# Performance work log

Hardware: AMD Instinct MI355X
Metric: run time of the kernel (lower is better)

Reference implementation:

```python
import jax, jax.numpy as jnp
import numpy as np

B, S, E, HEADS = 2, 2048, 2048, 16


def setup_inputs() -> dict:
    key = jax.random.key(0)
    k1, k2, k3 = jax.random.split(key, 3)
    x = jax.random.normal(k1, (B, S, E), dtype=jnp.float32)
    # Linear weights stored as (in, out); torch uses y = x @ W.T with W (out, in) -- same math.
    W_qkvh = jax.random.normal(k2, (E, 3 * E + HEADS), dtype=jnp.float32) * (E ** -0.5)
    W_out = jax.random.normal(k3, (E, E), dtype=jnp.float32) * (E ** -0.5)
    return {"x": x, "W_qkvh": W_qkvh, "W_out": W_out}


def reference(x, W_qkvh, W_out):
    b, s, e = x.shape
    heads = W_qkvh.shape[1] - 3 * e
    d = e // heads
    scale = e ** 0.5

    proj = x @ W_qkvh                                  # (b, s, 3e + heads)
    QKV, Hg = proj[..., : 3 * e], proj[..., 3 * e:]
    Hg = jnp.tanh(Hg).transpose(0, 2, 1)[..., None]    # (b, h, s, 1) gate
    QKV = QKV.reshape(b, s, heads, 3 * d).transpose(0, 2, 1, 3)  # (b, h, s, 3d)
    Q, K, V = jnp.split(QKV, 3, axis=-1)               # each (b, h, s, d)

    # Cummean(H*K) along seq: cumsum(n * x) / n^2 with n = 1..s
    n = jnp.arange(1, s + 1, dtype=x.dtype).reshape(1, 1, s, 1)
    Kc = jnp.cumsum(n * (Hg * K), axis=2) / (n * n)    # (b, h, s, d)

    scores = jnp.einsum('bhqd,bhkd->bhqk', Q, Kc) / scale
    causal = jnp.triu(jnp.ones((s, s), dtype=bool), k=1)
    scores = jnp.where(causal, -jnp.inf, scores)
    attn = jax.nn.softmax(scores, axis=-1)

    out = jnp.einsum('bhqk,bhkd->bhqd', attn, V)       # (b, h, s, d)
    out = out.transpose(0, 2, 1, 3).reshape(b, s, e)
    return out @ W_out
```

## Files before the change

kernel.cpp:

```cpp
#include <hip/hip_runtime.h>
#include <hip/hip_bf16.h>
#include <math.h>

#define PB 2
#define PS 2048
#define PE 2048
#define PH 16
#define PD 128
#define PN_PROJ 6160
#define PM 4096
#define PQKV 6144

typedef __attribute__((ext_vector_type(8))) short bf16x8;
typedef __attribute__((ext_vector_type(4))) float f32x4;

__device__ __forceinline__ void gload_lds16(const void* g, void* l) {
  __builtin_amdgcn_global_load_lds((const __attribute__((address_space(1))) void*)g,
                                   (__attribute__((address_space(3))) void*)l, 16, 0, 0);
}

template <int BM, int BN, int WM, int WN, typename OutT>
__global__ __launch_bounds__(512, 1) void gemm_cs2(
    const __hip_bfloat16* __restrict__ A, const __hip_bfloat16* __restrict__ Bt,
    OutT* __restrict__ C, int K, int lda, int ldb, int ldc, int nTilesX) {
  constexpr int MF = BM / WM / 16;
  constexpr int NF = BN / WN / 16;
  constexpr int SLOT = (BM + BN) * 64;
  constexpr int AL = BM / 64;
  constexpr int BL = BN / 64;
  constexpr int NLD = AL + BL;

  __shared__ __align__(16) __hip_bfloat16 lds[2 * SLOT];

  const int tid = threadIdx.x;
  const int w = tid >> 6, lane = tid & 63;
  const int fq = lane >> 4, fr = lane & 15;
  const int wm = w / WN, wn = w % WN;

  const int total = gridDim.x;
  const int swz = (blockIdx.x & 7) * (total >> 3) + (blockIdx.x >> 3);
  const int mBase = (swz / nTilesX) * BM;
  const int nBase = (swz % nTilesX) * BN;

  const int srow = tid >> 3, sc = tid & 7;

  auto stage = [&](int t) {
    char* base = (char*)lds + (size_t)(t & 1) * SLOT * 2;
#pragma unroll
    for (int l = 0; l < AL; ++l) {
      int row = l * 64 + srow;
      int cs = sc ^ (row & 7);
      gload_lds16(A + (size_t)(mBase + row) * lda + t * 64 + cs * 8,
                  base + l * 8192 + w * 1024);
    }
#pragma unroll
    for (int l = 0; l < BL; ++l) {
      int row = l * 64 + srow;
      int cs = sc ^ (row & 7);
      gload_lds16(Bt + (size_t)(nBase + row) * ldb + t * 64 + cs * 8,
                  base + BM * 128 + l * 8192 + w * 1024);
    }
  };

  f32x4 acc[MF][NF];
#pragma unroll
  for (int m = 0; m < MF; ++m)
#pragma unroll
    for (int n = 0; n < NF; ++n) acc[m][n] = (f32x4){0.f, 0.f, 0.f, 0.f};

  const int NT = K / 64;
  stage(0); stage(1);

#pragma unroll 1
  for (int t = 0; t < NT; ++t) {
    if (t + 1 < NT) asm volatile("s_waitcnt vmcnt(%0)" ::"i"(NLD) : "memory");
    else            asm volatile("s_waitcnt vmcnt(0)" ::: "memory");
    __builtin_amdgcn_s_barrier();
    __builtin_amdgcn_sched_barrier(0);

    const __hip_bfloat16* sl = lds + (size_t)(t & 1) * SLOT;

    bf16x8 av[MF], bv[NF];
#pragma unroll
    for (int m = 0; m < MF; ++m) {
      int row = wm * (BM / WM) + m * 16 + fr;
      av[m] = *(const bf16x8*)&sl[row * 64 + ((fq ^ (row & 7)) * 8)];
    }
#pragma unroll
    for (int n = 0; n < NF; ++n) {
      int row = wn * (BN / WN) + n * 16 + fr;
      bv[n] = *(const bf16x8*)&sl[BM * 64 + row * 64 + ((fq ^ (row & 7)) * 8)];
    }
    asm volatile("s_waitcnt lgkmcnt(0)" ::: "memory");
    __builtin_amdgcn_sched_barrier(0);
    __builtin_amdgcn_s_setprio(1);
#pragma unroll
    for (int m = 0; m < MF; ++m)
#pragma unroll
      for (int n = 0; n < NF; ++n)
        acc[m][n] = __builtin_amdgcn_mfma_f32_16x16x32_bf16(av[m], bv[n], acc[m][n], 0, 0, 0);
    __builtin_amdgcn_s_setprio(0);

#pragma unroll
    for (int m = 0; m < MF; ++m) {
      int row = wm * (BM / WM) + m * 16 + fr;
      av[m] = *(const bf16x8*)&sl[row * 64 + (((4 + fq) ^ (row & 7)) * 8)];
    }
#pragma unroll
    for (int n = 0; n < NF; ++n) {
      int row = wn * (BN / WN) + n * 16 + fr;
      bv[n] = *(const bf16x8*)&sl[BM * 64 + row * 64 + (((4 + fq) ^ (row & 7)) * 8)];
    }
    asm volatile("s_waitcnt lgkmcnt(0)" ::: "memory");
    __builtin_amdgcn_s_barrier();
    __builtin_amdgcn_sched_barrier(0);
    if (t + 2 < NT) stage(t + 2);
    __builtin_amdgcn_s_setprio(1);
#pragma unroll
    for (int m = 0; m < MF; ++m)
#pragma unroll
      for (int n = 0; n < NF; ++n)
        acc[m][n] = __builtin_amdgcn_mfma_f32_16x16x32_bf16(av[m], bv[n], acc[m][n], 0, 0, 0);
    __builtin_amdgcn_s_setprio(0);
  }

#pragma unroll
  for (int m = 0; m < MF; ++m) {
#pragma unroll
    for (int n = 0; n < NF; ++n) {
      int row0 = mBase + wm * (BM / WM) + m * 16 + fq * 4;
      int col = nBase + wn * (BN / WN) + n * 16 + fr;
#pragma unroll
      for (int j = 0; j < 4; ++j) {
        if constexpr (__is_same(OutT, float))
          C[(size_t)(row0 + j) * ldc + col] = acc[m][n][j];
        else
          C[(size_t)(row0 + j) * ldc + col] = __float2bfloat16(acc[m][n][j]);
      }
    }
  }
}

__global__ __launch_bounds__(256) void cast_f32_bf16(const float* __restrict__ in,
                                                     __hip_bfloat16* __restrict__ out,
                                                     int n4) {
  int i = blockIdx.x * 256 + threadIdx.x;
  if (i >= n4) return;
  float4 v = ((const float4*)in)[i];
  union { __hip_bfloat16 h[4]; uint2 u; } pk;
  pk.h[0] = __float2bfloat16(v.x); pk.h[1] = __float2bfloat16(v.y);
  pk.h[2] = __float2bfloat16(v.z); pk.h[3] = __float2bfloat16(v.w);
  ((uint2*)out)[i] = pk.u;
}

__global__ __launch_bounds__(256) void transpose_cast(const float* __restrict__ W,
                                                      __hip_bfloat16* __restrict__ Wt,
                                                      int ldw, int ldt, int nOff) {
  __shared__ float t[32][33];
  int nb = blockIdx.x * 32, kb = blockIdx.y * 32;
  int tx = threadIdx.x & 31, ty = threadIdx.x >> 5;
#pragma unroll
  for (int i = 0; i < 4; ++i) {
    int k = ty + i * 8;
    t[k][tx] = W[(size_t)(kb + k) * ldw + nOff + nb + tx];
  }
  __syncthreads();
#pragma unroll
  for (int i = 0; i < 4; ++i) {
    int n = ty + i * 8;
    Wt[(size_t)(nb + n) * ldt + kb + tx] = __float2bfloat16(t[tx][n]);
  }
}

__global__ __launch_bounds__(256) void hg_from_x(const float* __restrict__ x,
                                                 const float* __restrict__ W,
                                                 float* __restrict__ hgbuf) {
  int bs = blockIdx.x;
  int b = bs >> 11, s = bs & (PS - 1);
  __shared__ float xs[PE];
  __shared__ float red[16][17];
  const float* xr = x + (size_t)bs * PE;
  for (int i = threadIdx.x; i < PE / 4; i += 256)
    *(float4*)&xs[i * 4] = ((const float4*)xr)[i];
  __syncthreads();
  int h = threadIdx.x & 15, part = threadIdx.x >> 4;
  float acc = 0.f;
  for (int k = part * 128; k < part * 128 + 128; ++k)
    acc += xs[k] * W[(size_t)k * PN_PROJ + 3 * PE + h];
  red[part][h] = acc;
  __syncthreads();
  if (threadIdx.x < 16) {
    float sm = 0.f;
#pragma unroll
    for (int p = 0; p < 16; ++p) sm += red[p][threadIdx.x];
    hgbuf[(size_t)(b * PH + threadIdx.x) * PS + s] = tanhf(sm);
  }
}

#define KC_SCALE 0.022097086912079608f

__global__ __launch_bounds__(128) void kc_pass1(const __hip_bfloat16* __restrict__ proj,
                                                const float* __restrict__ hgbuf,
                                                float* __restrict__ csum) {
  int c = blockIdx.x & 15, bh = blockIdx.x >> 4;
  int h = bh & (PH - 1), b = bh >> 4;
  int d = threadIdx.x;
  __shared__ float hgs[128];
  hgs[d] = hgbuf[bh * PS + c * 128 + d];
  __syncthreads();
  const __hip_bfloat16* kbase = proj + (size_t)(b * PS) * PQKV + h * 384 + 128 + d;
  float acc = 0.f;
  int j0 = c * 128;
  for (int i = 0; i < 128; ++i) {
    int j = j0 + i;
    acc += (float)(j + 1) * hgs[i] * __bfloat162float(kbase[(size_t)j * PQKV]);
  }
  csum[blockIdx.x * 128 + d] = acc;
}

__global__ __launch_bounds__(128) void kc_pass2(__hip_bfloat16* __restrict__ proj,
                                                const float* __restrict__ hgbuf,
                                                const float* __restrict__ csum) {
  int c = blockIdx.x & 15, bh = blockIdx.x >> 4;
  int h = bh & (PH - 1), b = bh >> 4;
  int d = threadIdx.x;
  __shared__ float hgs[128];
  hgs[d] = hgbuf[bh * PS + c * 128 + d];
  __syncthreads();
  float acc = 0.f;
  for (int cc = 0; cc < c; ++cc) acc += csum[(bh * 16 + cc) * 128 + d];
  __hip_bfloat16* kbase = proj + (size_t)(b * PS) * PQKV + h * 384 + 128 + d;
  int j0 = c * 128;
  for (int i = 0; i < 128; ++i) {
    int j = j0 + i;
    acc += (float)(j + 1) * hgs[i] * __bfloat162float(kbase[(size_t)j * PQKV]);
    float t = (float)(j + 1);
    kbase[(size_t)j * PQKV] = __float2bfloat16(acc / (t * t) * KC_SCALE);
  }
}

__global__ __launch_bounds__(256) void vt_pack(const __hip_bfloat16* __restrict__ proj,
                                               __hip_bfloat16* __restrict__ Vtp) {
  int sc = blockIdx.x & 31, bh = blockIdx.x >> 5;
  int b = bh >> 4, h = bh & 15;
  int s0 = sc * 64;
  int tid = threadIdx.x;
  __shared__ __align__(16) __hip_bfloat16 Vlds[64][136];
  const __hip_bfloat16* src = proj + (size_t)(b * PS + s0) * PQKV + h * 384 + 256;
#pragma unroll
  for (int it = 0; it < 4; ++it) {
    int i = it * 256 + tid;
    int row = i >> 4, ch = i & 15;
    *(bf16x8*)&Vlds[row][ch * 8] = *(const bf16x8*)&src[(size_t)row * PQKV + ch * 8];
  }
  __syncthreads();
  int d = tid >> 1, half = tid & 1;
  __hip_bfloat16* dst = Vtp + ((size_t)bh * 128 + d) * PS + s0 + half * 32;
#pragma unroll
  for (int c8 = 0; c8 < 8; ++c8) {
    union { __hip_bfloat16 h4[4]; uint2 u; } pk;
#pragma unroll
    for (int k = 0; k < 4; ++k) pk.h4[k] = Vlds[half * 32 + c8 * 4 + k][d];
    *(uint2*)&dst[c8 * 4] = pk.u;
  }
}

__global__ __launch_bounds__(256) void attn_mfma(const __hip_bfloat16* __restrict__ proj,
                                                 const __hip_bfloat16* __restrict__ Vtp,
                                                 __hip_bfloat16* __restrict__ O) {
  const int bid = (blockIdx.x & 7) * 32 + (blockIdx.x >> 3);
  const int bh = bid >> 3, pk = bid & 7;
  const int b = bh >> 4, h = bh & 15;
  const int tid = threadIdx.x;
  const int w = tid >> 6, lane = tid & 63;
  const int fq = lane >> 4, fr = lane & 15;

  __shared__ __align__(16) char smem[120832];
  __hip_bfloat16* Psw = (__hip_bfloat16*)(smem + 65536) + w * 32 * 72;
  __hip_bfloat16* Os = (__hip_bfloat16*)(smem + 84480);

  const __hip_bfloat16* kb0 = proj + (size_t)(b * PS) * PQKV + h * 384 + 128;
  const __hip_bfloat16* vb0 = Vtp + (size_t)bh * 128 * PS;

  const int klr = lane >> 4, kc = lane & 15;
  const int vlr = lane >> 3, vc = lane & 7;

  auto stageKV = [&](int t, int bufi) {
    char* ksb = smem + bufi * 16384;
    char* vsb = smem + 32768 + bufi * 16384;
    const __hip_bfloat16* kb = kb0 + (size_t)(t * 64) * PQKV;
    const __hip_bfloat16* vb = vb0 + t * 64;
#pragma unroll
    for (int p = 0; p < 4; ++p) {
      int row = w * 16 + p * 4 + klr;
      int cs = kc ^ (row & 7);
      gload_lds16(kb + (size_t)row * PQKV + cs * 8, ksb + (w * 16 + p * 4) * 256);
    }
#pragma unroll
    for (int p = 0; p < 4; ++p) {
      int row = w * 32 + p * 8 + vlr;
      int cs = vc ^ (row & 7);
      gload_lds16(vb + (size_t)row * PS + cs * 8, vsb + (w * 32 + p * 8) * 128);
    }
  };

  stageKV(0, 0);
  int cur = 0;

#pragma unroll 1
  for (int phase = 0; phase < 2; ++phase) {
    const int qt = (phase == 0) ? pk : 15 - pk;
    const int nt = (qt + 1) * 2;
    const int q0 = qt * 128;
    const int qw = q0 + w * 32;

    const __hip_bfloat16* qbase = proj + (size_t)(b * PS + qw) * PQKV + h * 384;
    bf16x8 qf[2][4];
#pragma unroll
    for (int r2 = 0; r2 < 2; ++r2)
#pragma unroll
      for (int kk = 0; kk < 4; ++kk)
        qf[r2][kk] = *(const bf16x8*)&qbase[(size_t)(r2 * 16 + fr) * PQKV + kk * 32 + fq * 8];

    f32x4 oacc[2][8];
#pragma unroll
    for (int r2 = 0; r2 < 2; ++r2)
#pragma unroll
      for (int nd = 0; nd < 8; ++nd) oacc[r2][nd] = (f32x4){0.f, 0.f, 0.f, 0.f};
    float m_[2] = {-__builtin_inff(), -__builtin_inff()};
    float l_[2] = {0.f, 0.f};

#pragma unroll 1
    for (int kt = 0; kt < nt; ++kt) {
      const bool hasNext = (kt + 1 < nt) || (phase == 0);
      if (hasNext) stageKV((kt + 1 < nt) ? kt + 1 : 0, cur ^ 1);

      if (kt * 64 <= qw + 31) {
        const __hip_bfloat16* Ks = (const __hip_bfloat16*)(smem + cur * 16384);
        const __hip_bfloat16* Vts = (const __hip_bfloat16*)(smem + 32768 + cur * 16384);
        const bool diag = (kt * 64 + 63) > qw;

        f32x4 sacc[2][4];
#pragma unroll
        for (int r2 = 0; r2 < 2; ++r2)
#pragma unroll
          for (int n = 0; n < 4; ++n) sacc[r2][n] = (f32x4){0.f, 0.f, 0.f, 0.f};
#pragma unroll
        for (int kk = 0; kk < 4; ++kk) {
#pragma unroll
          for (int n = 0; n < 4; ++n) {
            bf16x8 kf = *(const bf16x8*)&Ks[(n * 16 + fr) * 128 + (((kk * 4 + fq) ^ (fr & 7)) * 8)];
            sacc[0][n] = __builtin_amdgcn_mfma_f32_16x16x32_bf16(kf, qf[0][kk], sacc[0][n], 0, 0, 0);
            sacc[1][n] = __builtin_amdgcn_mfma_f32_16x16x32_bf16(kf, qf[1][kk], sacc[1][n], 0, 0, 0);
          }
        }

#pragma unroll
        for (int r2 = 0; r2 < 2; ++r2) {
          const int qg = qw + r2 * 16 + fr;
          float sv[4][4];
#pragma unroll
          for (int n = 0; n < 4; ++n)
#pragma unroll
            for (int j = 0; j < 4; ++j) {
              float s = sacc[r2][n][j];
              if (diag && (kt * 64 + n * 16 + fq * 4 + j) > qg) s = -__builtin_inff();
              sv[n][j] = s;
            }
          float pmax = sv[0][0];
#pragma unroll
          for (int n = 0; n < 4; ++n)
#pragma unroll
            for (int j = 0; j < 4; ++j) pmax = fmaxf(pmax, sv[n][j]);
          pmax = fmaxf(pmax, __shfl_xor(pmax, 16, 64));
          pmax = fmaxf(pmax, __shfl_xor(pmax, 32, 64));

          const bool nof = __all(pmax <= m_[r2] + 8.f);
          const float mn = nof ? m_[r2] : fmaxf(m_[r2], pmax);
          float ps = 0.f;
#pragma unroll
          for (int n = 0; n < 4; ++n) {
            union { __hip_bfloat16 hh[4]; uint2 u; } pkk;
#pragma unroll
            for (int j = 0; j < 4; ++j) {
              float p = __expf(sv[n][j] - mn);
              ps += p;
              pkk.hh[j] = __float2bfloat16(p);
            }
            *(uint2*)&Psw[(r2 * 16 + fr) * 72 + n * 16 + fq * 4] = pkk.u;
          }
          ps += __shfl_xor(ps, 16, 64);
          ps += __shfl_xor(ps, 32, 64);

          if (!nof) {
            const float alpha = __expf(m_[r2] - mn);
            l_[r2] = l_[r2] * alpha + ps;
            m_[r2] = mn;
            float a0 = __shfl(alpha, fq * 4 + 0, 64);
            float a1 = __shfl(alpha, fq * 4 + 1, 64);
            float a2 = __shfl(alpha, fq * 4 + 2, 64);
            float a3 = __shfl(alpha, fq * 4 + 3, 64);
#pragma unroll
            for (int nd = 0; nd < 8; ++nd) {
              oacc[r2][nd][0] *= a0; oacc[r2][nd][1] *= a1;
              oacc[r2][nd][2] *= a2; oacc[r2][nd][3] *= a3;
            }
          } else {
            l_[r2] += ps;
          }
        }

#pragma unroll
        for (int kk2 = 0; kk2 < 2; ++kk2) {
          bf16x8 pa0 = *(const bf16x8*)&Psw[(0 * 16 + fr) * 72 + kk2 * 32 + fq * 8];
          bf16x8 pa1 = *(const bf16x8*)&Psw[(1 * 16 + fr) * 72 + kk2 * 32 + fq * 8];
#pragma unroll
          for (int nd = 0; nd < 8; ++nd) {
            bf16x8 vf = *(const bf16x8*)&Vts[(nd * 16 + fr) * 64 + (((kk2 * 4 + fq) ^ (fr & 7)) * 8)];
            oacc[0][nd] = __builtin_amdgcn_mfma_f32_16x16x32_bf16(pa0, vf, oacc[0][nd], 0, 0, 0);
            oacc[1][nd] = __builtin_amdgcn_mfma_f32_16x16x32_bf16(pa1, vf, oacc[1][nd], 0, 0, 0);
          }
        }
      }

      __syncthreads();
      cur ^= 1;
    }

    float i0 = 1.0f / l_[0], i1 = 1.0f / l_[1];
    float inv4[2][4];
#pragma unroll
    for (int j = 0; j < 4; ++j) {
      inv4[0][j] = __shfl(i0, fq * 4 + j, 64);
      inv4[1][j] = __shfl(i1, fq * 4 + j, 64);
    }
#pragma unroll
    for (int r2 = 0; r2 < 2; ++r2)
#pragma unroll
      for (int nd = 0; nd < 8; ++nd)
#pragma unroll
        for (int j = 0; j < 4; ++j)
          Os[(w * 32 + r2 * 16 + fq * 4 + j) * 136 + nd * 16 + fr] =
              __float2bfloat16(oacc[r2][nd][j] * inv4[r2][j]);
    __syncthreads();
#pragma unroll
    for (int it = 0; it < 8; ++it) {
      int i = it * 256 + tid;
      int row = i >> 4, ch = i & 15;
      *(bf16x8*)&O[(size_t)(b * PS + q0 + row) * PE + h * 128 + ch * 8] =
          *(const bf16x8*)&Os[row * 136 + ch * 8];
    }
  }
}

extern "C" void kernel_launch(void* const* d_in, const int* in_sizes, int n_in,
                              void* d_out, int out_size, void* d_ws, size_t ws_size,
                              hipStream_t stream) {
  const float* x     = (const float*)d_in[0];
  const float* Wqkvh = (const float*)d_in[1];
  const float* Wout  = (const float*)d_in[2];
  float* out = (float*)d_out;

  char* wsb = (char*)d_ws;
  __hip_bfloat16* proj = (__hip_bfloat16*)wsb;
  wsb += (size_t)PM * PQKV * 2;
  __hip_bfloat16* xb = (__hip_bfloat16*)wsb;
  wsb += (size_t)PM * PE * 2;
  __hip_bfloat16* Wq_t = (__hip_bfloat16*)wsb;
  wsb += (size_t)PQKV * PE * 2;
  __hip_bfloat16* Wout_t = (__hip_bfloat16*)wsb;
  wsb += (size_t)PE * PE * 2;
  __hip_bfloat16* Vtp = (__hip_bfloat16*)wsb;
  wsb += (size_t)PB * PH * PD * PS * 2;
  float* hgbuf = (float*)wsb;
  wsb += (size_t)PB * PH * PS * 4;
  float* csum = (float*)wsb;

  cast_f32_bf16<<<(PM * PE / 4 + 255) / 256, 256, 0, stream>>>(x, xb, PM * PE / 4);
  transpose_cast<<<dim3(PQKV / 32, PE / 32), 256, 0, stream>>>(Wqkvh, Wq_t, PN_PROJ, PE, 0);
  transpose_cast<<<dim3(PE / 32, PE / 32), 256, 0, stream>>>(Wout, Wout_t, PE, PE, 0);

  gemm_cs2<128, 384, 2, 4, __hip_bfloat16>
      <<<dim3((PM / 128) * (PQKV / 384)), 512, 0, stream>>>(
          xb, Wq_t, proj, PE, PE, PE, PQKV, PQKV / 384);

  hg_from_x<<<PM, 256, 0, stream>>>(x, Wqkvh, hgbuf);
  kc_pass1<<<PB * PH * 16, 128, 0, stream>>>(proj, hgbuf, csum);
  kc_pass2<<<PB * PH * 16, 128, 0, stream>>>(proj, hgbuf, csum);

  vt_pack<<<PB * PH * 32, 256, 0, stream>>>(proj, Vtp);
  __hip_bfloat16* Ob = xb;
  attn_mfma<<<PB * PH * 8, 256, 0, stream>>>(proj, Vtp, Ob);

  gemm_cs2<128, 256, 2, 4, float>
      <<<dim3((PM / 128) * (PE / 256)), 512, 0, stream>>>(
          Ob, Wout_t, out, PE, PE, PE, PE, PE / 256);
}
```

Baseline: 319.9 us.

## Enlarge QKV GEMM tile to 256x384 with 1024 threads and XCD-aware tile mapping

Generalizes the bf16 GEMM kernel to any thread count and moves the QKV projection to 256x384 tiles computed by 16 waves, which raises data reuse per tile and halves the block count. It also replaces the block-index swizzle with a mapping in which each XCD owns a contiguous group of N columns and walks M tiles, so weight tiles stay in that XCD's L2. The larger block uses more LDS and gives one wave per SIMD more work. With fewer blocks (256) the per-CU balance may get worse.

```diff
diff --git a/kernel.cpp b/kernel.cpp
--- a/kernel.cpp
+++ b/kernel.cpp
@@ -20,14 +20,16 @@
 }
 
 template <int BM, int BN, int WM, int WN, typename OutT>
-__global__ __launch_bounds__(512, 1) void gemm_cs2(
+__global__ __launch_bounds__(WM * WN * 64, 1) void gemm_cs2(
     const __hip_bfloat16* __restrict__ A, const __hip_bfloat16* __restrict__ Bt,
-    OutT* __restrict__ C, int K, int lda, int ldb, int ldc, int nTilesX) {
+    OutT* __restrict__ C, int K, int lda, int ldb, int ldc, int nTY, int nPerX) {
+  constexpr int T = WM * WN * 64;
   constexpr int MF = BM / WM / 16;
   constexpr int NF = BN / WN / 16;
   constexpr int SLOT = (BM + BN) * 64;
-  constexpr int AL = BM / 64;
-  constexpr int BL = BN / 64;
+  constexpr int RPR = T / 8;
+  constexpr int AL = BM / RPR;
+  constexpr int BL = BN / RPR;
   constexpr int NLD = AL + BL;
 
   __shared__ __align__(16) __hip_bfloat16 lds[2 * SLOT];
@@ -37,28 +39,29 @@
   const int fq = lane >> 4, fr = lane & 15;
   const int wm = w / WN, wn = w % WN;
 
-  const int total = gridDim.x;
-  const int swz = (blockIdx.x & 7) * (total >> 3) + (blockIdx.x >> 3);
-  const int mBase = (swz / nTilesX) * BM;
-  const int nBase = (swz % nTilesX) * BN;
+  const int xcd = blockIdx.x & 7;
+  const int local = blockIdx.x >> 3;
+  const int mBase = (local % nTY) * BM;
+  const int nBase = (xcd * nPerX + local / nTY) * BN;
 
   const int srow = tid >> 3, sc = tid & 7;
 
   auto stage = [&](int t) {
     char* base = (char*)lds + (size_t)(t & 1) * SLOT * 2;
+    const int wub16 = (tid & ~63) * 16;
 #pragma unroll
     for (int l = 0; l < AL; ++l) {
-      int row = l * 64 + srow;
+      int row = l * RPR + srow;
       int cs = sc ^ (row & 7);
       gload_lds16(A + (size_t)(mBase + row) * lda + t * 64 + cs * 8,
-                  base + l * 8192 + w * 1024);
+                  base + l * (T * 16) + wub16);
     }
 #pragma unroll
     for (int l = 0; l < BL; ++l) {
-      int row = l * 64 + srow;
+      int row = l * RPR + srow;
       int cs = sc ^ (row & 7);
       gload_lds16(Bt + (size_t)(nBase + row) * ldb + t * 64 + cs * 8,
-                  base + BM * 128 + l * 8192 + w * 1024);
+                  base + BM * 128 + l * (T * 16) + wub16);
     }
   };
 
@@ -480,9 +483,9 @@
   transpose_cast<<<dim3(PQKV / 32, PE / 32), 256, 0, stream>>>(Wqkvh, Wq_t, PN_PROJ, PE, 0);
   transpose_cast<<<dim3(PE / 32, PE / 32), 256, 0, stream>>>(Wout, Wout_t, PE, PE, 0);
 
-  gemm_cs2<128, 384, 2, 4, __hip_bfloat16>
-      <<<dim3((PM / 128) * (PQKV / 384)), 512, 0, stream>>>(
-          xb, Wq_t, proj, PE, PE, PE, PQKV, PQKV / 384);
+  gemm_cs2<256, 384, 4, 4, __hip_bfloat16>
+      <<<dim3((PM / 256) * (PQKV / 384)), 1024, 0, stream>>>(
+          xb, Wq_t, proj, PE, PE, PE, PQKV, PM / 256, (PQKV / 384) / 8);
 
   hg_from_x<<<PM, 256, 0, stream>>>(x, Wqkvh, hgbuf);
   kc_pass1<<<PB * PH * 16, 128, 0, stream>>>(proj, hgbuf, csum);
@@ -494,5 +497,5 @@
 
   gemm_cs2<128, 256, 2, 4, float>
       <<<dim3((PM / 128) * (PE / 256)), 512, 0, stream>>>(
-          Ob, Wout_t, out, PE, PE, PE, PE, PE / 256);
-}
+          Ob, Wout_t, out, PE, PE, PE, PE, PM / 128, (PE / 256) / 8);
+}
```

After: 586.0 us. 83.1% more time.
